# Kernel optimization log

Measured on AMD Instinct MI355X. Metric: run time of the kernel, lower is better.

The kernel has to match this reference:

```python
import jax, jax.numpy as jnp
import numpy as np

L, S, N, E = 2048, 2048, 4, 1024
FF = 4 * E


def _ln(x, g, b, eps=1e-5):
    m = jnp.mean(x, axis=-1, keepdims=True)
    v = jnp.mean((x - m) ** 2, axis=-1, keepdims=True)
    return (x - m) * jax.lax.rsqrt(v + eps) * g + b


def _attn(q_in, k_in, v_in, qw, kw, vw, in_b, ow, ob, mask):
    # q_in: [L,N,E], k_in/v_in: [S,N,E]; single head, head_dim == E
    e = q_in.shape[-1]
    scale = float(e) ** -0.5
    q = (q_in @ qw.T + in_b[:e]) * scale          # [L,N,E]
    k = k_in @ kw.T + in_b[e:2 * e]               # [S,N,E]
    v = v_in @ vw.T + in_b[2 * e:]                # [S,N,E]
    scores = jnp.einsum('lne,sne->nls', q, k)     # [N,L,S]
    if mask is not None:
        scores = scores + mask[None]
    w = jax.nn.softmax(scores, axis=-1)
    out = jnp.einsum('nls,sne->lne', w, v)        # [L,N,E]
    return out @ ow.T + ob


def setup_inputs() -> dict:
    key = jax.random.key(0)
    ks = jax.random.split(key, 24)
    g = lambda k, shape: jax.random.normal(k, shape, dtype=jnp.float32) * 0.02
    causal = jnp.where(jnp.triu(jnp.ones((L, L), dtype=bool), 1), -1e9, 0.0).astype(jnp.float32)
    return {
        'tgt': jax.random.normal(ks[0], (L, N, E), dtype=jnp.float32),
        'memory': jax.random.normal(ks[1], (S, N, E), dtype=jnp.float32),
        'tgt_mask': causal,
        'sa_qw': g(ks[2], (E, E)), 'sa_kw': g(ks[3], (E, E)), 'sa_vw': g(ks[4], (E, E)),
        'sa_b': jnp.zeros((3 * E,), jnp.float32),
        'sa_ow': g(ks[5], (E, E)), 'sa_ob': jnp.zeros((E,), jnp.float32),
        'ca_qw': g(ks[6], (E, E)), 'ca_kw': g(ks[7], (E, E)), 'ca_vw': g(ks[8], (E, E)),
        'ca_b': jnp.zeros((3 * E,), jnp.float32),
        'ca_ow': g(ks[9], (E, E)), 'ca_ob': jnp.zeros((E,), jnp.float32),
        'ln1_g': jnp.ones((E,), jnp.float32), 'ln1_b': jnp.zeros((E,), jnp.float32),
        'ln2_g': jnp.ones((E,), jnp.float32), 'ln2_b': jnp.zeros((E,), jnp.float32),
        'ln3_g': jnp.ones((E,), jnp.float32), 'ln3_b': jnp.zeros((E,), jnp.float32),
        'w1': g(ks[10], (FF, E)), 'b1': jnp.zeros((FF,), jnp.float32),
        'w2': g(ks[11], (E, FF)), 'b2': jnp.zeros((E,), jnp.float32),
    }


def reference(tgt, memory, tgt_mask,
              sa_qw, sa_kw, sa_vw, sa_b, sa_ow, sa_ob,
              ca_qw, ca_kw, ca_vw, ca_b, ca_ow, ca_ob,
              ln1_g, ln1_b, ln2_g, ln2_b, ln3_g, ln3_b,
              w1, b1, w2, b2):
    x = tgt
    # pre-norm self-attention with causal mask (dropout_p=0, eval)
    h = _ln(x, ln1_g, ln1_b)
    x = x + _attn(h, h, h, sa_qw, sa_kw, sa_vw, sa_b, sa_ow, sa_ob, tgt_mask)
    # pre-norm cross-attention over encoder memory
    h = _ln(x, ln2_g, ln2_b)
    x = x + _attn(h, memory, memory, ca_qw, ca_kw, ca_vw, ca_b, ca_ow, ca_ob, None)
    h = _ln(x, ln3_g, ln3_b)
    h = h @ w1.T + b1
    h = h * jax.nn.sigmoid(1.702 * h)
    x = x + (h @ w2.T + b2)
    return x
```

## Files before the change

kernel.cpp:

```cpp
#include <hip/hip_runtime.h>
#include <hip/hip_bf16.h>
#include <cstdint>
#include <cstddef>


using bf16_t = __bf16;
typedef __bf16 bf16x8 __attribute__((ext_vector_type(8)));
typedef __bf16 bf16x4 __attribute__((ext_vector_type(4)));
typedef float f32x4 __attribute__((ext_vector_type(4)));

__device__ __forceinline__ void gll16(const void* g, void* lds) {
  __builtin_amdgcn_global_load_lds(
      (__attribute__((address_space(1))) void*)(g),
      (__attribute__((address_space(3))) void*)(lds), 16, 0, 0);
}

__global__ __launch_bounds__(256) void f32_to_bf16_n(
    const float* __restrict__ in, bf16_t* __restrict__ out, int n) {
  const size_t i = ((size_t)blockIdx.x * 256 + threadIdx.x) * 8;
  if (i >= (size_t)n) return;
  f32x4 a = *(const f32x4*)(in + i);
  f32x4 b = *(const f32x4*)(in + i + 4);
  bf16x8 v;
#pragma unroll
  for (int j = 0; j < 4; ++j) { v[j] = (bf16_t)a[j]; v[4 + j] = (bf16_t)b[j]; }
  *(bf16x8*)(out + i) = v;
}

struct CastSeg { const float* src; bf16_t* dst; int chunks; };
struct CastDesc { CastSeg s[16]; };
__global__ __launch_bounds__(256) void cast_multi(CastDesc d) {
  int blk = blockIdx.x, seg = 0, base = 0;
  while (blk - base >= d.s[seg].chunks) { base += d.s[seg].chunks; ++seg; }
  const size_t i = (size_t)(blk - base) * 1024 + threadIdx.x * 4;
  f32x4 a = *(const f32x4*)(d.s[seg].src + i);
  bf16x4 v;
#pragma unroll
  for (int j = 0; j < 4; ++j) v[j] = (bf16_t)a[j];
  *(bf16x4*)(d.s[seg].dst + i) = v;
}

__global__ __launch_bounds__(256) void ln_kernel(
    const float* __restrict__ x, const float* __restrict__ g,
    const float* __restrict__ b, bf16_t* __restrict__ out) {
  const int row = blockIdx.x, tid = threadIdx.x;
  const float* xr = x + (size_t)row * 1024;
  float v0 = xr[tid], v1 = xr[tid + 256], v2 = xr[tid + 512], v3 = xr[tid + 768];
  float s = v0 + v1 + v2 + v3;
  float ss = v0 * v0 + v1 * v1 + v2 * v2 + v3 * v3;
#pragma unroll
  for (int off = 32; off > 0; off >>= 1) {
    s += __shfl_down(s, off, 64);
    ss += __shfl_down(ss, off, 64);
  }
  __shared__ float red[8];
  const int w = tid >> 6, lane = tid & 63;
  if (lane == 0) { red[w] = s; red[4 + w] = ss; }
  __syncthreads();
  s = red[0] + red[1] + red[2] + red[3];
  ss = red[4] + red[5] + red[6] + red[7];
  const float mean = s * (1.f / 1024.f);
  float var = ss * (1.f / 1024.f) - mean * mean;
  var = var < 0.f ? 0.f : var;
  const float inv = rsqrtf(var + 1e-5f);
  bf16_t* orow = out + (size_t)row * 1024;
  orow[tid]       = (bf16_t)((v0 - mean) * inv * g[tid]       + b[tid]);
  orow[tid + 256] = (bf16_t)((v1 - mean) * inv * g[tid + 256] + b[tid + 256]);
  orow[tid + 512] = (bf16_t)((v2 - mean) * inv * g[tid + 512] + b[tid + 512]);
  orow[tid + 768] = (bf16_t)((v3 - mean) * inv * g[tid + 768] + b[tid + 768]);
}

template <int CAUSAL>
__global__ __launch_bounds__(256) void softmax_kernel(bf16_t* __restrict__ sc) {
  const int row = blockIdx.x, tid = threadIdx.x;
  const int l = row & 2047;
  bf16_t* sr = sc + (size_t)row * 2048;
  float v[8];
  float mx = -3.4e38f;
#pragma unroll
  for (int i = 0; i < 8; ++i) {
    const int j = tid + i * 256;
    v[i] = (CAUSAL && j > l) ? -3.4e38f : (float)sr[j];
    mx = fmaxf(mx, v[i]);
  }
#pragma unroll
  for (int off = 32; off > 0; off >>= 1) mx = fmaxf(mx, __shfl_down(mx, off, 64));
  __shared__ float red[8];
  const int w = tid >> 6, lane = tid & 63;
  if (lane == 0) red[w] = mx;
  __syncthreads();
  mx = fmaxf(fmaxf(red[0], red[1]), fmaxf(red[2], red[3]));
  float sum = 0.f;
#pragma unroll
  for (int i = 0; i < 8; ++i) { v[i] = __expf(v[i] - mx); sum += v[i]; }
#pragma unroll
  for (int off = 32; off > 0; off >>= 1) sum += __shfl_down(sum, off, 64);
  if (lane == 0) red[4 + w] = sum;
  __syncthreads();
  sum = red[4] + red[5] + red[6] + red[7];
  const float r = 1.f / sum;
#pragma unroll
  for (int i = 0; i < 8; ++i) sr[tid + i * 256] = (bf16_t)(v[i] * r);
}

__global__ __launch_bounds__(256) void transpose_v(const bf16_t* __restrict__ v,
                                                   bf16_t* __restrict__ vt) {
  __shared__ bf16_t tile[64][72];
  const int n = blockIdx.z;
  const int s0 = blockIdx.x * 64, e0 = blockIdx.y * 64;
  const int tid = threadIdx.x;
#pragma unroll
  for (int j = 0; j < 2; ++j) {
    int flat = j * 256 + tid;
    int r = flat >> 3, c8 = (flat & 7) * 8;
    bf16x8 val = *(const bf16x8*)(v + ((size_t)(s0 + r) * 4 + n) * 1024 + e0 + c8);
#pragma unroll
    for (int i = 0; i < 8; ++i) tile[r][c8 + i] = val[i];
  }
  __syncthreads();
#pragma unroll
  for (int j = 0; j < 2; ++j) {
    int flat = j * 256 + tid;
    int er = flat >> 3, s8 = (flat & 7) * 8;
    bf16x8 val;
#pragma unroll
    for (int i = 0; i < 8; ++i) val[i] = tile[s8 + i][er];
    *(bf16x8*)(vt + ((size_t)n * 1024 + e0 + er) * 2048 + s0 + s8) = val;
  }
}

template <int EPI, int MODE, int NS>
__global__ __launch_bounds__(256) void gemm_bt(
    const bf16_t* __restrict__ A, const bf16_t* __restrict__ Aalt,
    long lda, long sA,
    const bf16_t* __restrict__ W0, const bf16_t* __restrict__ W1,
    const bf16_t* __restrict__ W2, long ldw, long sW,
    void* __restrict__ C0, void* __restrict__ C1, void* __restrict__ C2,
    long ldc, long sC,
    const bf16_t* __restrict__ bias, const float* __restrict__ res,
    float scale, int K) {
  const size_t row0 = (size_t)blockIdx.y * 128;
  const size_t col0 = (size_t)blockIdx.x * 128;
  if (MODE == 1 && col0 > row0) return;
  const int z = blockIdx.z;
  constexpr int BK = NS * 32;

  const bf16_t* Ap = (MODE == 3) ? (z == 0 ? A : Aalt) : A + (size_t)z * sA;
  const bf16_t* Wp = (MODE == 3) ? (z == 0 ? W0 : (z == 1 ? W1 : W2))
                                 : W0 + (size_t)z * sW;
  void* Cp = (MODE == 3) ? (z == 0 ? C0 : (z == 1 ? C1 : C2)) : C0;
  const size_t zoffC = (MODE == 3) ? 0 : (size_t)z * sC;
  const bf16_t* biasp = bias ? bias + (MODE == 3 ? z * 1024 : 0) : nullptr;
  const float scl = (MODE == 3 && z != 0) ? 1.f : scale;
  const int kend = (MODE == 2) ? min(K, (int)row0 + 128) : K;

  __shared__ __align__(16) bf16_t As[2][NS][128 * 32];
  __shared__ __align__(16) bf16_t Bs[2][NS][128 * 32];
  const int tid = threadIdx.x;
  const int wv = tid >> 6, lane = tid & 63;
  const int quad = lane >> 4, l15 = lane & 15;
  const int wr = wv >> 1, wc = wv & 1;

  const bf16_t* gA[2 * NS];
  const bf16_t* gW[2 * NS];
  int dof[2 * NS];
  const int soct = (lane & 3) ^ ((lane >> 3) & 3);
#pragma unroll
  for (int j = 0; j < 2 * NS; ++j) {
    const int c = wv * 2 * NS + j;
    const int ksc = c >> 3;
    const int rg = c & 7;
    const int rr = rg * 16 + (lane >> 2);
    const int cc = ksc * 32 + soct * 8;
    gA[j] = Ap + (row0 + rr) * lda + cc;
    gW[j] = Wp + (col0 + rr) * ldw + cc;
    dof[j] = ksc * 4096 + rg * 512;
  }

  f32x4 acc[4][4];
#pragma unroll
  for (int mi = 0; mi < 4; ++mi)
#pragma unroll
    for (int ni = 0; ni < 4; ++ni) acc[mi][ni] = (f32x4)0.f;

#pragma unroll
  for (int j = 0; j < 2 * NS; ++j) {
    gll16(gA[j], &As[0][0][0] + dof[j]);
    gll16(gW[j], &Bs[0][0][0] + dof[j]);
  }

  const int fro = l15 * 32 + (quad ^ ((l15 >> 1) & 3)) * 8;

  int p = 0;
  for (int k0 = 0; k0 < kend; k0 += BK, p ^= 1) {
    __syncthreads();
    const int kn = k0 + BK;
    if (kn < kend) {
#pragma unroll
      for (int j = 0; j < 2 * NS; ++j) {
        gll16(gA[j] + kn, &As[p ^ 1][0][0] + dof[j]);
        gll16(gW[j] + kn, &Bs[p ^ 1][0][0] + dof[j]);
      }
    }
#pragma unroll
    for (int ks = 0; ks < NS; ++ks) {
      bf16x8 af[4], bfv[4];
#pragma unroll
      for (int mi = 0; mi < 4; ++mi)
        af[mi] = *(const bf16x8*)(As[p][ks] + (wr * 4 + mi) * 512 + fro);
#pragma unroll
      for (int ni = 0; ni < 4; ++ni)
        bfv[ni] = *(const bf16x8*)(Bs[p][ks] + (wc * 4 + ni) * 512 + fro);
#pragma unroll
      for (int mi = 0; mi < 4; ++mi)
#pragma unroll
        for (int ni = 0; ni < 4; ++ni)
          acc[mi][ni] = __builtin_amdgcn_mfma_f32_16x16x32_bf16(
              af[mi], bfv[ni], acc[mi][ni], 0, 0, 0);
    }
  }

  float* Cf = (float*)Cp;
  bf16_t* Cb = (bf16_t*)Cp;
#pragma unroll
  for (int mi = 0; mi < 4; ++mi) {
    const size_t gr = row0 + wr * 64 + mi * 16 + quad * 4;
#pragma unroll
    for (int ni = 0; ni < 4; ++ni) {
      const size_t gc = col0 + wc * 64 + ni * 16 + l15;
      float bv = 0.f;
      if (EPI == 0 || EPI == 2 || EPI == 3) bv = biasp ? (float)biasp[gc] : 0.f;
#pragma unroll
      for (int r = 0; r < 4; ++r) {
        float v = acc[mi][ni][r];
        const size_t idx = zoffC + (gr + r) * ldc + gc;
        if (EPI == 0) {
          Cb[idx] = (bf16_t)((v + bv) * scl);
        } else if (EPI == 1) {
          Cb[idx] = (bf16_t)v;
        } else if (EPI == 2) {
          Cf[idx] = res[idx] + v + bv;
        } else {
          float t = v + bv;
          Cb[idx] = (bf16_t)(t * (1.f / (1.f + __expf(-1.702f * t))));
        }
      }
    }
  }
}

template <int EPI, int MODE>
__global__ __launch_bounds__(512, 2) void gemm256(
    const bf16_t* __restrict__ A, const bf16_t* __restrict__ Aalt,
    long lda, long sA,
    const bf16_t* __restrict__ W0, const bf16_t* __restrict__ W1,
    const bf16_t* __restrict__ W2, long ldw, long sW,
    void* __restrict__ C0, void* __restrict__ C1, void* __restrict__ C2,
    long ldc, long sC,
    const bf16_t* __restrict__ bias, float scale, int K) {
  const int gx = gridDim.x, gy = gridDim.y;
  const int nwg = gx * gy * (int)gridDim.z;
  const int hw = (int)blockIdx.x + gx * ((int)blockIdx.y + gy * (int)blockIdx.z);
  const int logical = (hw & 7) * (nwg >> 3) + (hw >> 3);
  const int bx = logical % gx;
  const int by = (logical / gx) % gy;
  const int z  = logical / (gx * gy);
  const size_t row0 = (size_t)by * 256, col0 = (size_t)bx * 256;
  if (MODE == 1 && bx > by) return;

  const bf16_t* Ap = (MODE == 3) ? (z == 0 ? A : Aalt) : A + (size_t)z * sA;
  const bf16_t* Wp = (MODE == 3) ? (z == 0 ? W0 : (z == 1 ? W1 : W2))
                                 : W0 + (size_t)z * sW;
  void* Cp = (MODE == 3) ? (z == 0 ? C0 : (z == 1 ? C1 : C2)) : C0;
  const size_t zoffC = (MODE == 3) ? 0 : (size_t)z * sC;
  const bf16_t* biasp = bias ? bias + (MODE == 3 ? z * 1024 : 0) : nullptr;
  const float scl = (MODE == 3 && z != 0) ? 1.f : scale;

  __shared__ __align__(16) bf16_t As[2][2][8192];
  __shared__ __align__(16) bf16_t Bs[2][2][8192];

  const int tid = threadIdx.x;
  const int lane = tid & 63, wid = tid >> 6;
  const int l15 = lane & 15, quad = lane >> 4;
  const int wm = wid >> 2, wn = wid & 3;

  const int soct = (lane & 3) ^ ((lane >> 3) & 3);
  const bf16_t* pA[2];
  const bf16_t* pB[2];
#pragma unroll
  for (int j = 0; j < 2; ++j) {
    const int rr = (wid * 2 + j) * 16 + (lane >> 2);
    const int kc = soct * 8;
    pA[j] = Ap + (row0 + rr) * lda + kc;
    pB[j] = Wp + (col0 + rr) * ldw + kc;
  }
  const int d0 = (wid * 2) * 512;
  const int d1 = (wid * 2 + 1) * 512;

  const int T = K >> 6;
  const int HT = 4 * T;

  auto stage = [&](int h) {
    if (h >= HT) return;
    const int u = h >> 2, ks = (h >> 1) & 1;
    const int coff = u * 64 + ks * 32;
    if (h & 1) {
      gll16(pB[0] + coff, &Bs[u & 1][ks][0] + d0);
      gll16(pB[1] + coff, &Bs[u & 1][ks][0] + d1);
    } else {
      gll16(pA[0] + coff, &As[u & 1][ks][0] + d0);
      gll16(pA[1] + coff, &As[u & 1][ks][0] + d1);
    }
  };

  f32x4 acc[2][4][4];
#pragma unroll
  for (int mh = 0; mh < 2; ++mh)
#pragma unroll
    for (int mi = 0; mi < 4; ++mi)
#pragma unroll
      for (int ni = 0; ni < 4; ++ni) acc[mh][mi][ni] = (f32x4)0.f;

#pragma unroll
  for (int h = 0; h < 6; ++h) stage(h);
  asm volatile("s_waitcnt vmcnt(8)" ::: "memory");
  __builtin_amdgcn_s_barrier();

  const int fro = l15 * 32 + (quad ^ ((l15 >> 1) & 3)) * 8;

  for (int t = 0; t < T; ++t) {
    const int p = t & 1;
    const int g4 = 4 * t;
    bf16x8 bfv[4];

#define PHASE(PH, KK, MH)                                                     \
    {                                                                         \
      bf16x8 af[4];                                                           \
      _Pragma("unroll")                                                       \
      for (int mi = 0; mi < 4; ++mi)                                          \
        af[mi] = *(const bf16x8*)(&As[p][KK][0] +                             \
                                  (wm * 8 + MH * 4 + mi) * 512 + fro);        \
      if (MH == 0) {                                                          \
        _Pragma("unroll")                                                     \
        for (int ni = 0; ni < 4; ++ni)                                        \
          bfv[ni] = *(const bf16x8*)(&Bs[p][KK][0] +                          \
                                     (wn * 4 + ni) * 512 + fro);              \
      }                                                                       \
      stage(g4 + 6 + PH);                                                     \
      if (PH == 0) {                                                          \
        if (t < T - 1) asm volatile("s_waitcnt vmcnt(2)" ::: "memory");       \
        else           asm volatile("s_waitcnt vmcnt(0)" ::: "memory");       \
      }                                                                       \
      __builtin_amdgcn_s_barrier();                                          \
      asm volatile("s_waitcnt lgkmcnt(0)" ::: "memory");                      \
      __builtin_amdgcn_sched_barrier(0);                                      \
      __builtin_amdgcn_s_setprio(1);                                         \
      _Pragma("unroll")                                                       \
      for (int mi = 0; mi < 4; ++mi)                                          \
        _Pragma("unroll")                                                     \
        for (int ni = 0; ni < 4; ++ni)                                        \
          acc[MH][mi][ni] = __builtin_amdgcn_mfma_f32_16x16x32_bf16(          \
              af[mi], bfv[ni], acc[MH][mi][ni], 0, 0, 0);                     \
      __builtin_amdgcn_s_setprio(0);                                          \
      __builtin_amdgcn_s_barrier();                                          \
    }

    PHASE(0, 0, 0)
    PHASE(1, 0, 1)
    PHASE(2, 1, 0)
    PHASE(3, 1, 1)
#undef PHASE
  }

  bf16_t* Cb = (bf16_t*)Cp;
#pragma unroll
  for (int mh = 0; mh < 2; ++mh)
#pragma unroll
    for (int mi = 0; mi < 4; ++mi) {
      const size_t gr = row0 + wm * 128 + mh * 64 + mi * 16 + quad * 4;
#pragma unroll
      for (int ni = 0; ni < 4; ++ni) {
        const size_t gc = col0 + wn * 64 + ni * 16 + l15;
        float bv = 0.f;
        if (EPI == 0 || EPI == 3) bv = biasp ? (float)biasp[gc] : 0.f;
#pragma unroll
        for (int r = 0; r < 4; ++r) {
          const float v = acc[mh][mi][ni][r];
          const size_t idx = zoffC + (gr + r) * ldc + gc;
          if (EPI == 0) {
            Cb[idx] = (bf16_t)((v + bv) * scl);
          } else if (EPI == 1) {
            Cb[idx] = (bf16_t)v;
          } else {
            const float tt = v + bv;
            Cb[idx] = (bf16_t)(tt * (1.f / (1.f + __expf(-1.702f * tt))));
          }
        }
      }
    }
}

template <int EPI, int MODE, int NS = 1>
static void launch_gemm(hipStream_t stream, int M, int N, int Z,
                        const void* A, const void* Aalt, long lda, long sA,
                        const void* W0, const void* W1, const void* W2,
                        long ldw, long sW,
                        void* C0, void* C1, void* C2, long ldc, long sC,
                        const void* bias, const float* res, float scale, int K) {
  dim3 grid(N / 128, M / 128, Z);
  gemm_bt<EPI, MODE, NS><<<grid, dim3(256), 0, stream>>>(
      (const bf16_t*)A, (const bf16_t*)Aalt, lda, sA,
      (const bf16_t*)W0, (const bf16_t*)W1, (const bf16_t*)W2, ldw, sW,
      C0, C1, C2, ldc, sC, (const bf16_t*)bias, res, scale, K);
}

template <int EPI, int MODE>
static void launch_gemm256(hipStream_t stream, int M, int N, int Z,
                           const void* A, const void* Aalt, long lda, long sA,
                           const void* W0, const void* W1, const void* W2,
                           long ldw, long sW,
                           void* C0, void* C1, void* C2, long ldc, long sC,
                           const void* bias, float scale, int K) {
  dim3 grid(N / 256, M / 256, Z);
  gemm256<EPI, MODE><<<grid, dim3(512), 0, stream>>>(
      (const bf16_t*)A, (const bf16_t*)Aalt, lda, sA,
      (const bf16_t*)W0, (const bf16_t*)W1, (const bf16_t*)W2, ldw, sW,
      C0, C1, C2, ldc, sC, (const bf16_t*)bias, scale, K);
}

extern "C" void kernel_launch(void* const* d_in, const int* in_sizes, int n_in,
                              void* d_out, int out_size, void* d_ws, size_t ws_size,
                              hipStream_t stream) {
  (void)in_sizes; (void)n_in; (void)out_size; (void)ws_size;
  const float* tgt  = (const float*)d_in[0];
  const float* mem  = (const float*)d_in[1];
  const float* sa_qw = (const float*)d_in[3];
  const float* sa_kw = (const float*)d_in[4];
  const float* sa_vw = (const float*)d_in[5];
  const float* sa_b  = (const float*)d_in[6];
  const float* sa_ow = (const float*)d_in[7];
  const float* sa_ob = (const float*)d_in[8];
  const float* ca_qw = (const float*)d_in[9];
  const float* ca_kw = (const float*)d_in[10];
  const float* ca_vw = (const float*)d_in[11];
  const float* ca_b  = (const float*)d_in[12];
  const float* ca_ow = (const float*)d_in[13];
  const float* ca_ob = (const float*)d_in[14];
  const float* ln1g = (const float*)d_in[15];
  const float* ln1b = (const float*)d_in[16];
  const float* ln2g = (const float*)d_in[17];
  const float* ln2b = (const float*)d_in[18];
  const float* ln3g = (const float*)d_in[19];
  const float* ln3b = (const float*)d_in[20];
  const float* w1 = (const float*)d_in[21];
  const float* b1 = (const float*)d_in[22];
  const float* w2 = (const float*)d_in[23];
  const float* b2 = (const float*)d_in[24];

  char* ws = (char*)d_ws;
  const size_t MB = 1048576;
  float*  xf   = (float*)(ws);
  bf16_t* hb   = (bf16_t*)(ws + 32 * MB);
  bf16_t* vb   = (bf16_t*)(ws + 48 * MB);
  bf16_t* qb   = (bf16_t*)(ws + 64 * MB);
  bf16_t* kb   = (bf16_t*)(ws + 80 * MB);
  bf16_t* vt   = (bf16_t*)(ws + 96 * MB);
  bf16_t* sb   = (bf16_t*)(ws + 32 * MB);
  bf16_t* ao   = kb;
  bf16_t* hid  = (bf16_t*)(ws + 48 * MB);
  bf16_t* memb = (bf16_t*)(ws + 112 * MB);
  bf16_t* wt   = (bf16_t*)(ws + 128 * MB);
  bf16_t* bb   = (bf16_t*)(ws + 160 * MB);

  const size_t M1 = 1048576;
  bf16_t* saq = wt,          *sak = wt + M1,     *sav = wt + 2 * M1;
  bf16_t* sao = wt + 3 * M1, *caq = wt + 4 * M1, *cak = wt + 5 * M1;
  bf16_t* cav = wt + 6 * M1, *cao = wt + 7 * M1;
  bf16_t* w1b = wt + 8 * M1;
  bf16_t* w2b = wt + 12 * M1;

  const float qscale = 0.03125f;

  CastDesc cd;
  auto seg = [&](int i, const float* s, bf16_t* d, int elems) {
    cd.s[i] = CastSeg{s, d, elems / 1024};
  };
  seg(0, sa_qw, saq, 1 << 20);  seg(1, sa_kw, sak, 1 << 20);
  seg(2, sa_vw, sav, 1 << 20);  seg(3, sa_ow, sao, 1 << 20);
  seg(4, ca_qw, caq, 1 << 20);  seg(5, ca_kw, cak, 1 << 20);
  seg(6, ca_vw, cav, 1 << 20);  seg(7, ca_ow, cao, 1 << 20);
  seg(8, w1, w1b, 1 << 22);     seg(9, w2, w2b, 1 << 22);
  seg(10, sa_b, bb, 3072);      seg(11, sa_ob, bb + 3072, 1024);
  seg(12, ca_b, bb + 4096, 3072); seg(13, ca_ob, bb + 7168, 1024);
  seg(14, b1, bb + 8192, 4096); seg(15, b2, bb + 12288, 1024);
  int total_chunks = 0;
  for (int i = 0; i < 16; ++i) total_chunks += cd.s[i].chunks;
  cast_multi<<<total_chunks, 256, 0, stream>>>(cd);
  f32_to_bf16_n<<<4096, 256, 0, stream>>>(mem, memb, 1 << 23);

  ln_kernel<<<8192, 256, 0, stream>>>(tgt, ln1g, ln1b, hb);
  launch_gemm256<0, 3>(stream, 8192, 1024, 3, hb, hb, 1024, 0,
                       saq, sak, sav, 1024, 0, qb, kb, vb, 1024, 0,
                       bb, qscale, 1024);
  transpose_v<<<dim3(32, 16, 4), 256, 0, stream>>>(vb, vt);
  launch_gemm256<1, 1>(stream, 2048, 2048, 4, qb, nullptr, 4096, 1024,
                       kb, nullptr, nullptr, 4096, 1024,
                       sb, nullptr, nullptr, 2048, 4194304, nullptr,
                       1.f, 1024);
  softmax_kernel<1><<<8192, 256, 0, stream>>>(sb);
  launch_gemm<0, 2, 2>(stream, 2048, 1024, 4, sb, nullptr, 2048, 4194304,
                       vt, nullptr, nullptr, 2048, 2097152,
                       ao, nullptr, nullptr, 4096, 1024, nullptr, nullptr,
                       1.f, 2048);
  launch_gemm<2, 0, 2>(stream, 8192, 1024, 1, ao, nullptr, 1024, 0,
                       sao, nullptr, nullptr, 1024, 0,
                       xf, nullptr, nullptr, 1024, 0, bb + 3072, tgt,
                       1.f, 1024);

  ln_kernel<<<8192, 256, 0, stream>>>(xf, ln2g, ln2b, hb);
  launch_gemm256<0, 3>(stream, 8192, 1024, 3, hb, memb, 1024, 0,
                       caq, cak, cav, 1024, 0, qb, kb, vb, 1024, 0,
                       bb + 4096, qscale, 1024);
  transpose_v<<<dim3(32, 16, 4), 256, 0, stream>>>(vb, vt);
  launch_gemm256<1, 0>(stream, 2048, 2048, 4, qb, nullptr, 4096, 1024,
                       kb, nullptr, nullptr, 4096, 1024,
                       sb, nullptr, nullptr, 2048, 4194304, nullptr,
                       1.f, 1024);
  softmax_kernel<0><<<8192, 256, 0, stream>>>(sb);
  launch_gemm<0, 0, 2>(stream, 2048, 1024, 4, sb, nullptr, 2048, 4194304,
                       vt, nullptr, nullptr, 2048, 2097152,
                       ao, nullptr, nullptr, 4096, 1024, nullptr, nullptr,
                       1.f, 2048);
  launch_gemm<2, 0, 2>(stream, 8192, 1024, 1, ao, nullptr, 1024, 0,
                       cao, nullptr, nullptr, 1024, 0,
                       xf, nullptr, nullptr, 1024, 0, bb + 7168, xf,
                       1.f, 1024);

  ln_kernel<<<8192, 256, 0, stream>>>(xf, ln3g, ln3b, hb);
  launch_gemm256<3, 0>(stream, 8192, 4096, 1, hb, nullptr, 1024, 0,
                       w1b, nullptr, nullptr, 1024, 0,
                       hid, nullptr, nullptr, 4096, 0, bb + 8192,
                       1.f, 1024);
  launch_gemm<2, 0, 2>(stream, 8192, 1024, 1, hid, nullptr, 4096, 0,
                       w2b, nullptr, nullptr, 4096, 0,
                       d_out, nullptr, nullptr, 1024, 0, bb + 12288, xf,
                       1.f, 4096);
}
```

Measured before the change: 807.2 us.

## Unroll GEMM main loops by two k-tiles with explicit per-phase staging and waits

Both bf16 GEMM kernels now unroll the K loop over pairs of tiles, so LDS buffer indices and global pointer offsets become compile-time constants advanced by pointer increments. The large kernel replaces the stage lambda with explicit per-phase load issue and hand-tuned vmcnt gates, and drops the per-phase lgkmcnt wait and sched_barrier. This is meant to cut address arithmetic and branch overhead and to let the compiler schedule LDS reads more freely. It assumes the K tile count is even, and hand-counted vmcnt values risk read-before-arrival bugs.

Measured after the change: 903.8 us. +12.0%, slower.

```diff
diff --git a/kernel.cpp b/kernel.cpp
--- a/kernel.cpp
+++ b/kernel.cpp
@@ -190,35 +190,50 @@
   }
 
   const int fro = l15 * 32 + (quad ^ ((l15 >> 1) & 3)) * 8;
-
-  int p = 0;
-  for (int k0 = 0; k0 < kend; k0 += BK, p ^= 1) {
+  const bf16_t* aR = &As[0][0][0] + wr * 2048 + fro;
+  const bf16_t* bR = &Bs[0][0][0] + wc * 2048 + fro;
+
+#define GBT_COMPUTE(P)                                                        \
+    _Pragma("unroll")                                                         \
+    for (int ks = 0; ks < NS; ++ks) {                                         \
+      bf16x8 af[4], bfv[4];                                                   \
+      _Pragma("unroll")                                                       \
+      for (int mi = 0; mi < 4; ++mi)                                          \
+        af[mi] = *(const bf16x8*)(aR + ((P)*NS + ks) * 4096 + mi * 512);      \
+      _Pragma("unroll")                                                       \
+      for (int ni = 0; ni < 4; ++ni)                                          \
+        bfv[ni] = *(const bf16x8*)(bR + ((P)*NS + ks) * 4096 + ni * 512);     \
+      _Pragma("unroll")                                                       \
+      for (int mi = 0; mi < 4; ++mi)                                          \
+        _Pragma("unroll")                                                     \
+        for (int ni = 0; ni < 4; ++ni)                                        \
+          acc[mi][ni] = __builtin_amdgcn_mfma_f32_16x16x32_bf16(              \
+              af[mi], bfv[ni], acc[mi][ni], 0, 0, 0);                         \
+    }
+
+  const int NP = kend / (2 * BK);
+  for (int pi = 0; pi < NP; ++pi) {
+    const bool morep = (pi < NP - 1);
     __syncthreads();
-    const int kn = k0 + BK;
-    if (kn < kend) {
+#pragma unroll
+    for (int j = 0; j < 2 * NS; ++j) {
+      gll16(gA[j] + BK, &As[0][0][0] + NS * 4096 + dof[j]);
+      gll16(gW[j] + BK, &Bs[0][0][0] + NS * 4096 + dof[j]);
+    }
+    GBT_COMPUTE(0)
+    __syncthreads();
+    if (morep) {
 #pragma unroll
       for (int j = 0; j < 2 * NS; ++j) {
-        gll16(gA[j] + kn, &As[p ^ 1][0][0] + dof[j]);
-        gll16(gW[j] + kn, &Bs[p ^ 1][0][0] + dof[j]);
+        gll16(gA[j] + 2 * BK, &As[0][0][0] + dof[j]);
+        gll16(gW[j] + 2 * BK, &Bs[0][0][0] + dof[j]);
       }
     }
-#pragma unroll
-    for (int ks = 0; ks < NS; ++ks) {
-      bf16x8 af[4], bfv[4];
-#pragma unroll
-      for (int mi = 0; mi < 4; ++mi)
-        af[mi] = *(const bf16x8*)(As[p][ks] + (wr * 4 + mi) * 512 + fro);
-#pragma unroll
-      for (int ni = 0; ni < 4; ++ni)
-        bfv[ni] = *(const bf16x8*)(Bs[p][ks] + (wc * 4 + ni) * 512 + fro);
-#pragma unroll
-      for (int mi = 0; mi < 4; ++mi)
-#pragma unroll
-        for (int ni = 0; ni < 4; ++ni)
-          acc[mi][ni] = __builtin_amdgcn_mfma_f32_16x16x32_bf16(
-              af[mi], bfv[ni], acc[mi][ni], 0, 0, 0);
-    }
-  }
+    GBT_COMPUTE(1)
+#pragma unroll
+    for (int j = 0; j < 2 * NS; ++j) { gA[j] += 2 * BK; gW[j] += 2 * BK; }
+  }
+#undef GBT_COMPUTE
 
   float* Cf = (float*)Cp;
   bf16_t* Cb = (bf16_t*)Cp;
@@ -285,33 +300,24 @@
   const int wm = wid >> 2, wn = wid & 3;
 
   const int soct = (lane & 3) ^ ((lane >> 3) & 3);
-  const bf16_t* pA[2];
-  const bf16_t* pB[2];
-#pragma unroll
-  for (int j = 0; j < 2; ++j) {
-    const int rr = (wid * 2 + j) * 16 + (lane >> 2);
-    const int kc = soct * 8;
-    pA[j] = Ap + (row0 + rr) * lda + kc;
-    pB[j] = Wp + (col0 + rr) * ldw + kc;
-  }
+  const int rr0 = (wid * 2) * 16 + (lane >> 2);
+  const int rr1 = (wid * 2 + 1) * 16 + (lane >> 2);
+  const bf16_t* pA0 = Ap + (row0 + rr0) * lda + soct * 8;
+  const bf16_t* pA1 = Ap + (row0 + rr1) * lda + soct * 8;
+  const bf16_t* pB0 = Wp + (col0 + rr0) * ldw + soct * 8;
+  const bf16_t* pB1 = Wp + (col0 + rr1) * ldw + soct * 8;
   const int d0 = (wid * 2) * 512;
   const int d1 = (wid * 2 + 1) * 512;
 
   const int T = K >> 6;
-  const int HT = 4 * T;
-
-  auto stage = [&](int h) {
-    if (h >= HT) return;
-    const int u = h >> 2, ks = (h >> 1) & 1;
-    const int coff = u * 64 + ks * 32;
-    if (h & 1) {
-      gll16(pB[0] + coff, &Bs[u & 1][ks][0] + d0);
-      gll16(pB[1] + coff, &Bs[u & 1][ks][0] + d1);
-    } else {
-      gll16(pA[0] + coff, &As[u & 1][ks][0] + d0);
-      gll16(pA[1] + coff, &As[u & 1][ks][0] + d1);
-    }
-  };
+  const int TP = T >> 1;
+
+#define SGA(OFF, PU, KS)                                                      \
+    do { gll16(pA0 + (OFF), &As[PU][KS][0] + d0);                             \
+         gll16(pA1 + (OFF), &As[PU][KS][0] + d1); } while (0)
+#define SGB(OFF, PU, KS)                                                      \
+    do { gll16(pB0 + (OFF), &Bs[PU][KS][0] + d0);                             \
+         gll16(pB1 + (OFF), &Bs[PU][KS][0] + d1); } while (0)
 
   f32x4 acc[2][4][4];
 #pragma unroll
@@ -321,39 +327,31 @@
 #pragma unroll
       for (int ni = 0; ni < 4; ++ni) acc[mh][mi][ni] = (f32x4)0.f;
 
-#pragma unroll
-  for (int h = 0; h < 6; ++h) stage(h);
+  SGA(0, 0, 0);  SGB(0, 0, 0);
+  SGA(32, 0, 1); SGB(32, 0, 1);
+  SGA(64, 1, 0); SGB(64, 1, 0);
   asm volatile("s_waitcnt vmcnt(8)" ::: "memory");
   __builtin_amdgcn_s_barrier();
 
   const int fro = l15 * 32 + (quad ^ ((l15 >> 1) & 3)) * 8;
-
-  for (int t = 0; t < T; ++t) {
-    const int p = t & 1;
-    const int g4 = 4 * t;
-    bf16x8 bfv[4];
-
-#define PHASE(PH, KK, MH)                                                     \
+  const bf16_t* aP = &As[0][0][0] + wm * 4096 + fro;
+  const bf16_t* bP = &Bs[0][0][0] + wn * 2048 + fro;
+
+#define PH(POFF, KK, MH, STAGE, GATE)                                         \
     {                                                                         \
       bf16x8 af[4];                                                           \
       _Pragma("unroll")                                                       \
       for (int mi = 0; mi < 4; ++mi)                                          \
-        af[mi] = *(const bf16x8*)(&As[p][KK][0] +                             \
-                                  (wm * 8 + MH * 4 + mi) * 512 + fro);        \
+        af[mi] = *(const bf16x8*)(aP + (POFF) + (KK) * 8192 +                 \
+                                  ((MH) * 4 + mi) * 512);                     \
       if (MH == 0) {                                                          \
         _Pragma("unroll")                                                     \
         for (int ni = 0; ni < 4; ++ni)                                        \
-          bfv[ni] = *(const bf16x8*)(&Bs[p][KK][0] +                          \
-                                     (wn * 4 + ni) * 512 + fro);              \
+          bfv[ni] = *(const bf16x8*)(bP + (POFF) + (KK) * 8192 + ni * 512);   \
       }                                                                       \
-      stage(g4 + 6 + PH);                                                     \
-      if (PH == 0) {                                                          \
-        if (t < T - 1) asm volatile("s_waitcnt vmcnt(2)" ::: "memory");       \
-        else           asm volatile("s_waitcnt vmcnt(0)" ::: "memory");       \
-      }                                                                       \
+      STAGE;                                                                  \
+      GATE;                                                                   \
       __builtin_amdgcn_s_barrier();                                          \
-      asm volatile("s_waitcnt lgkmcnt(0)" ::: "memory");                      \
-      __builtin_amdgcn_sched_barrier(0);                                      \
       __builtin_amdgcn_s_setprio(1);                                         \
       _Pragma("unroll")                                                       \
       for (int mi = 0; mi < 4; ++mi)                                          \
@@ -365,12 +363,28 @@
       __builtin_amdgcn_s_barrier();                                          \
     }
 
-    PHASE(0, 0, 0)
-    PHASE(1, 0, 1)
-    PHASE(2, 1, 0)
-    PHASE(3, 1, 1)
-#undef PHASE
-  }
+  for (int pi = 0; pi < TP; ++pi) {
+    const bool more = (pi < TP - 1);
+    bf16x8 bfv[4];
+    PH(0, 0, 0, SGA(96, 1, 1),
+       asm volatile("s_waitcnt vmcnt(6)" ::: "memory"))
+    PH(0, 0, 1, SGB(96, 1, 1), )
+    PH(0, 1, 0, if (more) SGA(128, 0, 0), )
+    PH(0, 1, 1, if (more) SGB(128, 0, 0),
+       if (more) asm volatile("s_waitcnt vmcnt(8)" ::: "memory");
+       else      asm volatile("s_waitcnt vmcnt(4)" ::: "memory"))
+    PH(16384, 0, 0, if (more) SGA(160, 0, 1),
+       if (more) asm volatile("s_waitcnt vmcnt(6)" ::: "memory");
+       else      asm volatile("s_waitcnt vmcnt(0)" ::: "memory"))
+    PH(16384, 0, 1, if (more) SGB(160, 0, 1), )
+    PH(16384, 1, 0, if (more) SGA(192, 1, 0), )
+    PH(16384, 1, 1, if (more) SGB(192, 1, 0),
+       if (more) asm volatile("s_waitcnt vmcnt(8)" ::: "memory"))
+    pA0 += 128; pA1 += 128; pB0 += 128; pB1 += 128;
+  }
+#undef PH
+#undef SGA
+#undef SGB
 
   bf16_t* Cb = (bf16_t*)Cp;
 #pragma unroll
```
